# Kernel tuning notes

Hardware: AMD Instinct MI355X
Metric: run time of the kernel (lower is better)

Reference implementation:

```python
import jax, jax.numpy as jnp
import numpy as np

EPS = 1e-6
POWER_ITERS = 5
B, S, D, H, HD, M = 4, 1024, 1024, 16, 64, 2736
SOFTCAP = 50.0


def _rms_norm(x, scale, eps=EPS):
    # flax RMSNorm: normalize in fp32 over last axis, then scale
    x32 = x.astype(jnp.float32)
    y = x32 * jax.lax.rsqrt(jnp.mean(x32 * x32, axis=-1, keepdims=True) + eps)
    return (y * scale).astype(x.dtype)


def _spectral_sigma(k2d, power_iters=POWER_ITERS, eps=EPS):
    u = jnp.ones((k2d.shape[1],), dtype=k2d.dtype)
    u = u / (jnp.linalg.norm(u) + eps)

    def body(_, u):
        v = jax.lax.stop_gradient(k2d @ u)
        v = v / (jnp.linalg.norm(v) + eps)
        u = jax.lax.stop_gradient(k2d.T @ v)
        u = u / (jnp.linalg.norm(u) + eps)
        return u

    u = jax.lax.fori_loop(0, power_iters, body, u)
    v = jax.lax.stop_gradient(k2d @ u)
    v = v / (jnp.linalg.norm(v) + eps)
    sigma = jnp.einsum('i,ij,j->', v, k2d, u)
    return jnp.maximum(sigma, eps)


def _sigma_dense(x, kernel, sigma_p, bias):
    # spectral-normalized dense; kernel may be (in, out) or (in, H, HD)
    k2d = kernel.reshape(kernel.shape[0], -1)
    sigma = _spectral_sigma(k2d)
    k_hat = (sigma_p / sigma) * kernel  # sigma_p shape (1,)
    y = jnp.tensordot(x, k_hat, axes=[[-1], [0]])
    return y + bias


def setup_inputs() -> dict:
    key = jax.random.key(0)
    ks = jax.random.split(key, 16)

    def kinit(k, shape, fan_in):
        return jax.random.normal(k, shape, jnp.float32) / np.sqrt(fan_in)

    one = jnp.ones((1,), jnp.float32)
    return {
        'x': jax.random.normal(ks[0], (B, S, D), jnp.float32),
        'ln1_scale': jnp.ones((D,), jnp.float32),
        'wq': kinit(ks[1], (D, H, HD), D), 'sq': one, 'bq': jnp.zeros((H, HD), jnp.float32),
        'wk': kinit(ks[2], (D, H, HD), D), 'sk': one, 'bk': jnp.zeros((H, HD), jnp.float32),
        'wv': kinit(ks[3], (D, H, HD), D), 'sv': one, 'bv': jnp.zeros((H, HD), jnp.float32),
        'qn_scale': jnp.ones((HD,), jnp.float32),
        'kn_scale': jnp.ones((HD,), jnp.float32),
        'wo': kinit(ks[4], (D, D), D), 'so': one, 'bo': jnp.zeros((D,), jnp.float32),
        'ln2_scale': jnp.ones((D,), jnp.float32),
        'wg': kinit(ks[5], (D, M), D), 'sg': one, 'bg': jnp.zeros((M,), jnp.float32),
        'wu': kinit(ks[6], (D, M), D), 'su': one, 'bu': jnp.zeros((M,), jnp.float32),
        'wd': kinit(ks[7], (M, D), M), 'sd': one, 'bd': jnp.zeros((D,), jnp.float32),
    }


def reference(x, ln1_scale, wq, sq, bq, wk, sk, bk, wv, sv, bv,
              qn_scale, kn_scale, wo, so, bo, ln2_scale,
              wg, sg, bg, wu, su, bu, wd, sd, bd):
    # --- attention ---
    attn_in = _rms_norm(x, ln1_scale)
    q = _sigma_dense(attn_in, wq, sq, bq)  # [B,S,H,HD]
    k = _sigma_dense(attn_in, wk, sk, bk)
    v = _sigma_dense(attn_in, wv, sv, bv)
    q = _rms_norm(q, qn_scale)
    k = _rms_norm(k, kn_scale)
    scale = jnp.sqrt(jnp.float32(HD))
    logits = jnp.einsum('bqhd,bkhd->bhqk', q, k) / scale
    logits = SOFTCAP * jnp.tanh(logits / SOFTCAP)
    attn = jax.nn.softmax(logits, axis=-1)
    out = jnp.einsum('bhqk,bkhd->bqhd', attn, v).reshape(B, S, D)
    out = _sigma_dense(out, wo, so, bo)
    x = x + out
    # --- gated MLP (swiglu) ---
    mlp_in = _rms_norm(x, ln2_scale)
    gate = _sigma_dense(mlp_in, wg, sg, bg)
    up = _sigma_dense(mlp_in, wu, su, bu)
    mlp = jax.nn.silu(gate) * up
    mlp = _sigma_dense(mlp, wd, sd, bd)
    return x + mlp
```

## Files before the change

### kernel.cpp

```cpp
#include <hip/hip_runtime.h>
#include <math.h>
#include <stddef.h>
#include <stdint.h>

#define BB   4
#define SS   1024
#define DD   1024
#define HH   16
#define HDD  64
#define NT   (BB*SS)
#define MFF  2736
#define MFFP 2752
#define EPSF 1e-6f

typedef unsigned int   u32;
typedef unsigned short ushort_t;
typedef float  f32x4   __attribute__((ext_vector_type(4)));
typedef float  f32x16  __attribute__((ext_vector_type(16)));
typedef short  s16x8   __attribute__((ext_vector_type(8)));

typedef const __attribute__((address_space(1))) u32 glb_u32;
typedef __attribute__((address_space(3))) u32 lds_u32;

static const size_t OFF_X2    = 0;
static const size_t OFF_VT    = 4194304;
static const size_t OFF_QH    = 8388608;
static const size_t OFF_O     = 16777216;
static const size_t OFF_H     = 8388608;
static const size_t OFF_ACT   = 26607616;
static const size_t OFF_POOL  = 30801920;
static const size_t OFF_VV    = 36569088;
static const size_t OFF_UU    = 36588240;
static const size_t OFF_SCALE = 36607392;

__device__ inline ushort_t f2bf(float x){
  u32 u = __float_as_uint(x);
  u32 r = (u + 0x7fffu + ((u >> 16) & 1u)) >> 16;
  return (ushort_t)r;
}
__device__ inline void split_bf(float x, ushort_t& hi, ushort_t& lo){
  hi = f2bf(x);
  float hf = __uint_as_float(((u32)hi) << 16);
  lo = f2bf(x - hf);
}
__device__ inline float bf2f(ushort_t u){
  return __uint_as_float(((u32)u) << 16);
}
__device__ inline s16x8 mk8(u32 a, u32 b, u32 c, u32 d){
  union { u32 w[4]; s16x8 v; } u;
  u.w[0]=a; u.w[1]=b; u.w[2]=c; u.w[3]=d;
  return u.v;
}

__device__ inline float block_sum256(float v, float* red){
  #pragma unroll
  for (int off=32; off>=1; off>>=1) v += __shfl_down(v, off);
  int lane = threadIdx.x & 63, wave = threadIdx.x >> 6;
  if (lane == 0) red[wave] = v;
  __syncthreads();
  return red[0]+red[1]+red[2]+red[3];
}

struct W2Args { const float* W[7]; ushort_t* dst; };
__global__ __launch_bounds__(256) void w2bf(W2Args a){
  const int BST[8] = {0,512,1024,1536,2048,3416,4784,6152};
  const size_t OFFU[7] = {0,1048576,2097152,3145728,4194304,6995968,9797632};
  int blk = blockIdx.x; int m = 0;
  #pragma unroll
  for (int i=1;i<7;i++) if (blk >= BST[i]) m = i;
  size_t e = (size_t)(blk - BST[m])*2048 + threadIdx.x*8;
  const float* src = a.W[m] + e;
  float4 v0 = *(const float4*)src;
  float4 v1 = *(const float4*)(src + 4);
  union { ushort_t o[8]; s16x8 v; } u;
  u.o[0]=f2bf(v0.x); u.o[1]=f2bf(v0.y); u.o[2]=f2bf(v0.z); u.o[3]=f2bf(v0.w);
  u.o[4]=f2bf(v1.x); u.o[5]=f2bf(v1.y); u.o[6]=f2bf(v1.z); u.o[7]=f2bf(v1.w);
  *(s16x8*)(a.dst + OFFU[m] + e) = u.v;
}

struct PowArgs {
  const ushort_t* Wb;
  float* vvec; float* uvec; int step;
};

__global__ __launch_bounds__(256) void zero_uvec(float* uvec){
  int m = blockIdx.x;
  for (int i=threadIdx.x; i<2736; i+=256) uvec[m*2736+i] = 0.f;
}

__global__ __launch_bounds__(256) void mv_notrans(PowArgs pa){
  const int NIN [7] = {1024,1024,1024,1024,1024,1024,2736};
  const int NOUT[7] = {1024,1024,1024,1024,2736,2736,1024};
  const int BST [8] = {0,256,512,768,1024,1280,1536,2220};
  const size_t OFFU[7] = {0,1048576,2097152,3145728,4194304,6995968,9797632};
  __shared__ float red[4];
  int blk = blockIdx.x;
  int m = 0;
  #pragma unroll
  for (int i=1;i<7;i++) if (blk >= BST[i]) m = i;
  int nin = NIN[m], nout = NOUT[m];
  int st = pa.step;
  float inv;
  const float* x = pa.uvec + m*2736;
  if (st == 0){
    inv = 1.f/(sqrtf((float)nout)+EPSF);
  } else {
    float s = 0.f;
    for (int i=threadIdx.x; i<nout; i+=256){ float u = x[i]; s += u*u; }
    float tot = block_sum256(s, red);
    inv = 1.f/(sqrtf(tot)+EPSF);
  }
  int wave = threadIdx.x >> 6, lane = threadIdx.x & 63;
  int row = (blk - BST[m])*4 + wave;
// ... 23 lines not shown
}

__global__ __launch_bounds__(256) void mv_trans(PowArgs pa){
  const int NIN [7] = {1024,1024,1024,1024,1024,1024,2736};
  const int NOUT[7] = {1024,1024,1024,1024,2736,2736,1024};
  const int BST [8] = {0,32,64,96,128,216,304,392};
  const int RCH [7] = {8,8,8,8,8,8,22};
  const size_t OFFU[7] = {0,1048576,2097152,3145728,4194304,6995968,9797632};
  __shared__ float red[4];
  int blk = blockIdx.x;
  int m = 0;
  #pragma unroll
  for (int i=1;i<7;i++) if (blk >= BST[i]) m = i;
  int nin = NIN[m], nout = NOUT[m];
  const float* v = pa.vvec + m*2736;
  float s = 0.f;
  for (int i=threadIdx.x; i<nin; i+=256){ float t = v[i]; s += t*t; }
  float tot = block_sum256(s, red);
  float inv = 1.f/(sqrtf(tot)+EPSF);
  int local = blk - BST[m];
  int ct = local / RCH[m], rc = local % RCH[m];
  int col = ct*256 + threadIdx.x;
  int r0 = rc*128, r1 = min(nin, r0+128);
  if (col >= nout) return;
  const ushort_t* W = pa.Wb + OFFU[m];
  float partial = 0.f;
  for (int r=r0; r<r1; ++r)
    partial += bf2f(W[(size_t)r*nout + col])*(v[r]*inv);
  atomicAdd(&pa.uvec[m*2736+col], partial);
}

struct SigArgs {
  const float* vvec; float* scale;
  const float* sp[7];
};
__global__ __launch_bounds__(256) void sigma_scale_kernel(SigArgs sa){
  const int NIN [7] = {1024,1024,1024,1024,1024,1024,2736};
  __shared__ float red[4];
  int m = blockIdx.x;
  const float* v = sa.vvec + m*2736;
  float s = 0.f;
  for (int i=threadIdx.x; i<NIN[m]; i+=256){ float t = v[i]; s += t*t; }
  float a = block_sum256(s, red);
  if (threadIdx.x == 0){
    float S = sqrtf(a);
    float sig = a/(S+EPSF);
    sig = fmaxf(sig, EPSF);
    sa.scale[m] = sa.sp[m][0]/sig;
  }
}

struct TCArgs {
  const float* src0; const float* src1;
  ushort_t* dh; ushort_t* dl;
  size_t zoff; int K; int N; int Kpad;
};
__global__ __launch_bounds__(256) void trans_cvt2(TCArgs a){
  __shared__ float t[32][33];
  const float* src = blockIdx.z ? a.src1 : a.src0;
  ushort_t* dh = a.dh + blockIdx.z*a.zoff;
  ushort_t* dl = a.dl + blockIdx.z*a.zoff;
  int k0 = blockIdx.x*32, n0 = blockIdx.y*32;
  int c = threadIdx.x & 31, rb = threadIdx.x >> 5;
  #pragma unroll
  for (int i=0;i<4;i++){
    int r = rb + i*8;
    int kk = k0 + r, nn = n0 + c;
    t[r][c] = (kk<a.K && nn<a.N) ? src[(size_t)kk*a.N + nn] : 0.f;
  }
  __syncthreads();
  #pragma unroll
  for (int i=0;i<4;i++){
    int r = rb + i*8;
    int nn = n0 + r, kk = k0 + c;
    float v = t[c][r];
    ushort_t hi, lo; split_bf(v, hi, lo);
    size_t o = (size_t)nn*a.Kpad + kk;
    dh[o] = hi; dl[o] = lo;
  }
}

__global__ __launch_bounds__(256) void rms_cvt(const float* __restrict__ in,
                                               const float* __restrict__ scale,
                                               ushort_t* __restrict__ oh,
                                               ushort_t* __restrict__ ol){
  int row = blockIdx.x;
  int tid = threadIdx.x;
  const float* p = in + (size_t)row*DD;
  float4 vx = *(const float4*)(p + tid*4);
  float ss = vx.x*vx.x + vx.y*vx.y + vx.z*vx.z + vx.w*vx.w;
  int lane = tid & 63, wave = tid >> 6;
  #pragma unroll
  for (int off=32; off>=1; off>>=1) ss += __shfl_down(ss, off);
  __shared__ float red[4];
  if (lane == 0) red[wave] = ss;
  __syncthreads();
  float tot = red[0]+red[1]+red[2]+red[3];
  float r = rsqrtf(tot*(1.f/DD)+EPSF);
  float4 sc = *(const float4*)(scale + tid*4);
  float o0 = vx.x*r*sc.x, o1 = vx.y*r*sc.y, o2 = vx.z*r*sc.z, o3 = vx.w*r*sc.w;
  ushort_t h[4], l[4];
  split_bf(o0,h[0],l[0]); split_bf(o1,h[1],l[1]);
  split_bf(o2,h[2],l[2]); split_bf(o3,h[3],l[3]);
  size_t o = (size_t)row*DD + tid*4;
  oh[o+0]=h[0]; oh[o+1]=h[1]; oh[o+2]=h[2]; oh[o+3]=h[3];
  ol[o+0]=l[0]; ol[o+1]=l[1]; ol[o+2]=l[2]; ol[o+3]=l[3];
}

struct GemmArgs {
  const ushort_t *Ah, *Al, *Bh, *Bl;
  float* C;
  const float *bias0, *bias1;
  const float *nrm0, *nrm1;
  ushort_t *dH0, *dL0, *dH1, *dL1;
  const float* scaleBase;
  const float* resid;
  int Kd, matN, bpm, rowsPerMat, Cstride, colOff;
};

template<int FN, int EPI>
__global__ __launch_bounds__(256) void gemm_bf3(GemmArgs g){
  constexpr int BN   = FN*32;
  constexpr int SEGB = BN/16;
  constexpr int NSEG = 16 + 2*SEGB;
  constexpr int NSEGT = NSEG/4;
  constexpr int HALF = 16384 + 2*BN*64;
  __shared__ __align__(16) char lds[2*HALF];

  const int tid = threadIdx.x;
  const int w = tid >> 6, l = tid & 63;
  const int bm = blockIdx.y*128;
  const int mat = blockIdx.x / g.bpm;
  const int n0m = (blockIdx.x % g.bpm) * BN;
  const int nrow0 = mat*g.rowsPerMat + n0m;

  const ushort_t* sp[NSEGT];
  u32 loff[NSEGT];
  #pragma unroll
  for (int i=0;i<NSEGT;i++){
    int s = w + i*4;
    int ci, r, c, csrc;
    if (s < 16){
      int abuf = s >> 3, segi = s & 7;
      ci = segi*64 + l; r = ci >> 2; c = ci & 3;
      csrc = c ^ ((r >> 1) & 3);
      sp[i] = (abuf ? g.Al : g.Ah) + (size_t)(bm + r)*g.Kd + csrc*8;
      loff[i] = (u32)(abuf*8192 + ci*16);
    } else {
      int tt = s - 16;
      int bbuf = tt / SEGB, segi = tt % SEGB;
      ci = segi*64 + l; r = ci >> 2; c = ci & 3;
      csrc = c ^ ((r >> 1) & 3);
      sp[i] = (bbuf ? g.Bl : g.Bh) + (size_t)(nrow0 + r)*g.Kd + csrc*8;
      loff[i] = (u32)(16384 + bbuf*(BN*64) + ci*16);
    }
  }

  const int wm = w >> 1, wn = w & 1;
  const int li = l & 15, kq = l >> 4;
  const int sx = kq ^ ((li >> 1) & 3);
  const u32 aOff = (u32)((wm*64 + li)*64 + sx*16);
  const u32 bOff = (u32)(16384 + (wn*(FN*16) + li)*64 + sx*16);

  f32x4 acc[4][FN];
  #pragma unroll
  for (int mi=0;mi<4;mi++)
    #pragma unroll
    for (int ni=0;ni<FN;ni++)
      acc[mi][ni] = (f32x4){0.f,0.f,0.f,0.f};

  const int nt = g.Kd >> 5;
  #pragma unroll
  for (int i=0;i<NSEGT;i++){
    __builtin_amdgcn_global_load_lds((glb_u32*)sp[i], (lds_u32*)(lds + loff[i]), 16, 0, 0);
    sp[i] += 32;
  }
  __syncthreads();

  for (int t=0; t<nt; t++){
    if (t+1 < nt){
      char* sb = lds + ((t+1)&1)*HALF;
      #pragma unroll
      for (int i=0;i<NSEGT;i++){
        __builtin_amdgcn_global_load_lds((glb_u32*)sp[i], (lds_u32*)(sb + loff[i]), 16, 0, 0);
        sp[i] += 32;
      }
    }
    const char* lb = lds + (t&1)*HALF;
    s16x8 ah[4], al[4];
    #pragma unroll
    for (int mi=0;mi<4;mi++){
      ah[mi] = *(const s16x8*)(lb + aOff + mi*1024);
      al[mi] = *(const s16x8*)(lb + 8192 + aOff + mi*1024);
    }
    #pragma unroll
    for (int ni=0;ni<FN;ni++){
      s16x8 bh = *(const s16x8*)(lb + bOff + ni*1024);
      s16x8 bl = *(const s16x8*)(lb + BN*64 + bOff + ni*1024);
      #pragma unroll
      for (int mi=0;mi<4;mi++){
        f32x4 tacc = acc[mi][ni];
        tacc = __builtin_amdgcn_mfma_f32_16x16x32_bf16(ah[mi], bh, tacc, 0, 0, 0);
        tacc = __builtin_amdgcn_mfma_f32_16x16x32_bf16(ah[mi], bl, tacc, 0, 0, 0);
        tacc = __builtin_amdgcn_mfma_f32_16x16x32_bf16(al[mi], bh, tacc, 0, 0, 0);
        acc[mi][ni] = tacc;
      }
    }
    __syncthreads();
  }

  if constexpr (EPI == 0){
    const float s = g.scaleBase[mat];
    const float* bias = g.bias0;
    const int colBase = n0m + wn*(FN*16);
    #pragma unroll
    for (int ni=0;ni<FN;ni++){
      int cm = colBase + ni*16 + li;
      if (cm < g.matN){
        int cg = cm + g.colOff;
        float bv = bias[cm];
        #pragma unroll
        for (int mi=0;mi<4;mi++){
          f32x4 a = acc[mi][ni];
          int r0 = bm + wm*64 + mi*16 + kq*4;
          #pragma unroll
          for (int j=0;j<4;j++){
            float v = s*a[j] + bv;
            size_t off = (size_t)(r0+j)*g.Cstride + cg;
            if (g.resid) v += g.resid[off];
            g.C[off] = v;
          }
        }
      }
    }
  } else if constexpr (EPI == 1){
    const float s = g.scaleBase[mat];
    const float* bias = mat ? g.bias1 : g.bias0;
    const float* nsc  = mat ? g.nrm1  : g.nrm0;
    ushort_t* dH = mat ? g.dH1 : g.dH0;
    ushort_t* dL = mat ? g.dL1 : g.dL0;
    const int hidx = (n0m >> 6) + wn;
    float bv[FN], nv[FN];
    #pragma unroll
    for (int ni=0;ni<FN;ni++){
      int cm = n0m + wn*64 + ni*16 + li;
      bv[ni] = bias[cm];
      nv[ni] = nsc[ni*16 + li];
    }
    #pragma unroll
    for (int mi=0;mi<4;mi++){
      #pragma unroll
      for (int j=0;j<4;j++){
        float vv[FN]; float ssq = 0.f;
        #pragma unroll
        for (int ni=0;ni<FN;ni++){
          vv[ni] = s*acc[mi][ni][j] + bv[ni];
          ssq += vv[ni]*vv[ni];
        }
        ssq += __shfl_xor(ssq, 1);
        ssq += __shfl_xor(ssq, 2);
        ssq += __shfl_xor(ssq, 4);
        ssq += __shfl_xor(ssq, 8);
        float rr = rsqrtf(ssq*(1.f/64.f)+EPSF);
        int row = bm + wm*64 + mi*16 + kq*4 + j;
        size_t base = (((size_t)(row>>10)*16 + hidx)*1024 + (row & 1023))*64;
        #pragma unroll
        for (int ni=0;ni<FN;ni++){
          ushort_t hi, lo; split_bf(vv[ni]*rr*nv[ni], hi, lo);
          dH[base + ni*16 + li] = hi;
          dL[base + ni*16 + li] = lo;
        }
      }
    }
  } else {
    const float s = g.scaleBase[0];
    #pragma unroll
    for (int mi=0;mi<4;mi++){
      #pragma unroll
      for (int j=0;j<4;j++){
        int row = bm + wm*64 + mi*16 + kq*4 + j;
        float bvr = g.bias0[row];
        #pragma unroll
        for (int ni=0;ni<FN;ni++){
          int cm = n0m + wn*(FN*16) + ni*16 + li;
          float v = s*acc[mi][ni][j] + bvr;
          ushort_t hi, lo; split_bf(v, hi, lo);
          g.dH0[(size_t)row*4096 + cm] = hi;
          g.dL0[(size_t)row*4096 + cm] = lo;
        }
      }
    }
  }
}

struct GluArgs {
  const ushort_t *Ah, *Al;
  const ushort_t *GH, *GL, *UH, *UL;
  const float *bg, *bu;
  const float* scaleBase;
  ushort_t *hH, *hL;
};

__global__ __launch_bounds__(256) void gemm_glu(GluArgs g){
  constexpr int HALF = 32768;
  __shared__ __align__(16) char lds[2*HALF];
  const int tid = threadIdx.x;
  const int w = tid >> 6, l = tid & 63;
  const int bm = blockIdx.y*128;
  const int n0 = blockIdx.x*64;

  const ushort_t* sp[8];
  u32 loff[8];
  #pragma unroll
  for (int i=0;i<8;i++){
    int s = w + i*4;
    if (s < 16){
      int abuf = s >> 3, segi = s & 7;
      int ci = segi*64 + l, r = ci >> 2, c = ci & 3;
      int csrc = c ^ ((r >> 1) & 3);
      sp[i] = (abuf ? g.Al : g.Ah) + (size_t)(bm + r)*1024 + csrc*8;
      loff[i] = (u32)(abuf*8192 + ci*16);
    } else {
      int tt = s - 16;
      int msel = tt >> 3;
      int half = (tt >> 2) & 1;
      int segi = tt & 3;
      int ci = segi*64 + l, r = ci >> 2, c = ci & 3;
      int csrc = c ^ ((r >> 1) & 3);
      const ushort_t* base = msel ? (half ? g.UL : g.UH) : (half ? g.GL : g.GH);
      sp[i] = base + (size_t)(n0 + r)*1024 + csrc*8;
      loff[i] = (u32)(16384 + msel*8192 + half*4096 + ci*16);
    }
  }

  const int wm = w >> 1, wn = w & 1;
  const int li = l & 15, kq = l >> 4;
  const int sx = kq ^ ((li >> 1) & 3);
  const u32 aOff = (u32)((wm*64 + li)*64 + sx*16);
  const u32 bOff = (u32)(16384 + (wn*32 + li)*64 + sx*16);

  f32x4 accG[4][2], accU[4][2];
  #pragma unroll
  for (int mi=0;mi<4;mi++)
    #pragma unroll
    for (int ni=0;ni<2;ni++){
      accG[mi][ni] = (f32x4){0.f,0.f,0.f,0.f};
      accU[mi][ni] = (f32x4){0.f,0.f,0.f,0.f};
    }

  #pragma unroll
  for (int i=0;i<8;i++){
    __builtin_amdgcn_global_load_lds((glb_u32*)sp[i], (lds_u32*)(lds + loff[i]), 16, 0, 0);
    sp[i] += 32;
  }
  __syncthreads();

  for (int t=0; t<32; t++){
    if (t+1 < 32){
      char* sb = lds + ((t+1)&1)*HALF;
      #pragma unroll
      for (int i=0;i<8;i++){
        __builtin_amdgcn_global_load_lds((glb_u32*)sp[i], (lds_u32*)(sb + loff[i]), 16, 0, 0);
        sp[i] += 32;
      }
    }
    const char* lb = lds + (t&1)*HALF;
    s16x8 ah[4], al[4];
    #pragma unroll
    for (int mi=0;mi<4;mi++){
      ah[mi] = *(const s16x8*)(lb + aOff + mi*1024);
      al[mi] = *(const s16x8*)(lb + 8192 + aOff + mi*1024);
    }
    #pragma unroll
    for (int ni=0;ni<2;ni++){
      s16x8 gh = *(const s16x8*)(lb + bOff + ni*1024);
      s16x8 gl = *(const s16x8*)(lb + 4096 + bOff + ni*1024);
      s16x8 uh = *(const s16x8*)(lb + 8192 + bOff + ni*1024);
      s16x8 ul = *(const s16x8*)(lb + 12288 + bOff + ni*1024);
      #pragma unroll
      for (int mi=0;mi<4;mi++){
        f32x4 tg = accG[mi][ni];
        tg = __builtin_amdgcn_mfma_f32_16x16x32_bf16(ah[mi], gh, tg, 0, 0, 0);
        tg = __builtin_amdgcn_mfma_f32_16x16x32_bf16(ah[mi], gl, tg, 0, 0, 0);
        tg = __builtin_amdgcn_mfma_f32_16x16x32_bf16(al[mi], gh, tg, 0, 0, 0);
        accG[mi][ni] = tg;
        f32x4 tu = accU[mi][ni];
        tu = __builtin_amdgcn_mfma_f32_16x16x32_bf16(ah[mi], uh, tu, 0, 0, 0);
        tu = __builtin_amdgcn_mfma_f32_16x16x32_bf16(ah[mi], ul, tu, 0, 0, 0);
        tu = __builtin_amdgcn_mfma_f32_16x16x32_bf16(al[mi], uh, tu, 0, 0, 0);
        accU[mi][ni] = tu;
      }
    }
    __syncthreads();
  }

  const float sG = g.scaleBase[0], sU = g.scaleBase[1];
  #pragma unroll
  for (int ni=0;ni<2;ni++){
    int cm = n0 + wn*32 + ni*16 + li;
    bool ok = cm < MFF;
    float bgv = ok ? g.bg[cm] : 0.f;
    float buv = ok ? g.bu[cm] : 0.f;
    #pragma unroll
    for (int mi=0;mi<4;mi++){
      #pragma unroll
      for (int j=0;j<4;j++){
        int row = bm + wm*64 + mi*16 + kq*4 + j;
        ushort_t hb = 0, lb2 = 0;
        if (ok){
          float gv = sG*accG[mi][ni][j] + bgv;
          float uv = sU*accU[mi][ni][j] + buv;
          float hv = gv * __builtin_amdgcn_rcpf(1.f + __expf(-gv)) * uv;
          split_bf(hv, hb, lb2);
        }
        size_t ho = (size_t)row*MFFP + cm;
        g.hH[ho] = hb; g.hL[ho] = lb2;
      }
    }
  }
}

__global__ __launch_bounds__(256) void attn_mfma(const ushort_t* __restrict__ qh, const ushort_t* __restrict__ ql,
                                                 const ushort_t* __restrict__ kh, const ushort_t* __restrict__ kl,
                                                 const ushort_t* __restrict__ vh, const ushort_t* __restrict__ vl,
                                                 ushort_t* __restrict__ oh, ushort_t* __restrict__ ol){
  __shared__ __align__(16) char lds[74240];
  const int qt = blockIdx.x, h = blockIdx.y, b = blockIdx.z;
  const int tid = threadIdx.x;
  const int l = tid & 63, li = tid & 31, hi = (tid >> 5) & 1;
  const int w = tid >> 6, qhalf = w >> 1, khalf = w & 1;
  const int r0 = tid >> 3, ch = tid & 7;

  const size_t qrow = ((size_t)(b*HH + h)*SS + qt*64 + qhalf*32 + li)*64;
  s16x8 aQh[4], aQl[4];
  #pragma unroll
  for (int ks=0; ks<4; ks++){
    aQh[ks] = *(const s16x8*)(qh + qrow + ks*16 + hi*8);
    aQl[ks] = *(const s16x8*)(ql + qrow + ks*16 + hi*8);
  }

  const size_t kbase = (size_t)(b*HH + h)*SS*64;
  const size_t vbase = (size_t)h*64*4096 + (size_t)b*SS;

  f32x16 accO0 = (f32x16){0,0,0,0,0,0,0,0,0,0,0,0,0,0,0,0};
  f32x16 accO1 = (f32x16){0,0,0,0,0,0,0,0,0,0,0,0,0,0,0,0};
  float psum = 0.f;

  s16x8 rKh0,rKh1,rKl0,rKl1,rVh0,rVh1,rVl0,rVl1;
  rKh0 = *(const s16x8*)(kh + kbase + (size_t)r0*64 + ch*8);
  rKh1 = *(const s16x8*)(kh + kbase + (size_t)(r0+32)*64 + ch*8);
  rKl0 = *(const s16x8*)(kl + kbase + (size_t)r0*64 + ch*8);
  rKl1 = *(const s16x8*)(kl + kbase + (size_t)(r0+32)*64 + ch*8);
  rVh0 = *(const s16x8*)(vh + vbase + (size_t)r0*4096 + ch*8);
  rVh1 = *(const s16x8*)(vh + vbase + (size_t)(r0+32)*4096 + ch*8);
  rVl0 = *(const s16x8*)(vl + vbase + (size_t)r0*4096 + ch*8);
  rVl1 = *(const s16x8*)(vl + vbase + (size_t)(r0+32)*4096 + ch*8);
  {
    char* Kb = lds;  char* Vb = lds + 36864;
    *(s16x8*)(Kb + r0*144 + ch*16) = rKh0;
    *(s16x8*)(Kb + (r0+32)*144 + ch*16) = rKh1;
    *(s16x8*)(Kb + 9216 + r0*144 + ch*16) = rKl0;
    *(s16x8*)(Kb + 9216 + (r0+32)*144 + ch*16) = rKl1;
    *(s16x8*)(Vb + r0*144 + ch*16) = rVh0;
    *(s16x8*)(Vb + (r0+32)*144 + ch*16) = rVh1;
    *(s16x8*)(Vb + 9216 + r0*144 + ch*16) = rVl0;
    *(s16x8*)(Vb + 9216 + (r0+32)*144 + ch*16) = rVl1;
  }
  __syncthreads();

  int cur = 0;
  for (int kt=0; kt<16; kt++){
    if (kt < 15){
      const size_t kb = kbase + (size_t)(kt+1)*64*64;
      const size_t vb = vbase + (size_t)(kt+1)*64;
      rKh0 = *(const s16x8*)(kh + kb + (size_t)r0*64 + ch*8);
      rKh1 = *(const s16x8*)(kh + kb + (size_t)(r0+32)*64 + ch*8);
      rKl0 = *(const s16x8*)(kl + kb + (size_t)r0*64 + ch*8);
      rKl1 = *(const s16x8*)(kl + kb + (size_t)(r0+32)*64 + ch*8);
      rVh0 = *(const s16x8*)(vh + vb + (size_t)r0*4096 + ch*8);
      rVh1 = *(const s16x8*)(vh + vb + (size_t)(r0+32)*4096 + ch*8);
      rVl0 = *(const s16x8*)(vl + vb + (size_t)r0*4096 + ch*8);
      rVl1 = *(const s16x8*)(vl + vb + (size_t)(r0+32)*4096 + ch*8);
    }
    const char* Kc = lds + cur*18432;
    const char* Vc = lds + 36864 + cur*18432;

    f32x16 sF = (f32x16){0,0,0,0,0,0,0,0,0,0,0,0,0,0,0,0};
    #pragma unroll
    for (int ks=0; ks<4; ks++){
      s16x8 kfh = *(const s16x8*)(Kc + (khalf*32+li)*144 + ks*32 + hi*16);
      s16x8 kfl = *(const s16x8*)(Kc + 9216 + (khalf*32+li)*144 + ks*32 + hi*16);
      sF = __builtin_amdgcn_mfma_f32_32x32x16_bf16(kfh, aQh[ks], sF, 0, 0, 0);
      sF = __builtin_amdgcn_mfma_f32_32x32x16_bf16(kfl, aQh[ks], sF, 0, 0, 0);
      sF = __builtin_amdgcn_mfma_f32_32x32x16_bf16(kfh, aQl[ks], sF, 0, 0, 0);
    }

    float p[16];
    #pragma unroll
    for (int r=0; r<16; r++){
      float wv = __expf(sF[r]*0.005f);
      float rc = __builtin_amdgcn_rcpf(wv + 1.f);
      float pv = __expf(-100.f*rc);
      p[r] = pv;
      psum += pv;
    }

    u32 cH[8], cL[8];
    #pragma unroll
    for (int m=0; m<4; m++){
      u32 u0 = __float_as_uint(p[4*m+0]), u1 = __float_as_uint(p[4*m+1]);
      u32 u2 = __float_as_uint(p[4*m+2]), u3 = __float_as_uint(p[4*m+3]);
      u32 m0 = u0 & 0xffff0000u, m1 = u1 & 0xffff0000u;
      u32 m2 = u2 & 0xffff0000u, m3 = u3 & 0xffff0000u;
      cH[2*m+0] = m1 | (m0 >> 16);
      cH[2*m+1] = m3 | (m2 >> 16);
      u32 k0 = __float_as_uint(p[4*m+0] - __uint_as_float(m0));
      u32 k1 = __float_as_uint(p[4*m+1] - __uint_as_float(m1));
      u32 k2 = __float_as_uint(p[4*m+2] - __uint_as_float(m2));
      u32 k3 = __float_as_uint(p[4*m+3] - __uint_as_float(m3));
      cL[2*m+0] = (k1 & 0xffff0000u) | (k0 >> 16);
      cL[2*m+1] = (k3 & 0xffff0000u) | (k2 >> 16);
    }

    #pragma unroll
    for (int ks2=0; ks2<2; ks2++){
      u32 A0 = cH[4*ks2+0], A1 = cH[4*ks2+1], B0 = cH[4*ks2+2], B1 = cH[4*ks2+3];
      u32 As0 = (u32)__shfl_xor((int)A0, 32), As1 = (u32)__shfl_xor((int)A1, 32);
      u32 Bs0 = (u32)__shfl_xor((int)B0, 32), Bs1 = (u32)__shfl_xor((int)B1, 32);
      s16x8 paH = mk8(hi ? Bs0 : A0, hi ? Bs1 : A1, hi ? B0 : As0, hi ? B1 : As1);
      u32 C0 = cL[4*ks2+0], C1 = cL[4*ks2+1], D0 = cL[4*ks2+2], D1 = cL[4*ks2+3];
      u32 Cs0 = (u32)__shfl_xor((int)C0, 32), Cs1 = (u32)__shfl_xor((int)C1, 32);
      u32 Ds0 = (u32)__shfl_xor((int)D0, 32), Ds1 = (u32)__shfl_xor((int)D1, 32);
      s16x8 paL = mk8(hi ? Ds0 : C0, hi ? Ds1 : C1, hi ? D0 : Cs0, hi ? D1 : Cs1);

      {
        const char* vp = Vc + (0*32+li)*144 + khalf*64 + ks2*32 + hi*16;
        s16x8 vfh = *(const s16x8*)vp;
        s16x8 vfl = *(const s16x8*)(vp + 9216);
        accO0 = __builtin_amdgcn_mfma_f32_32x32x16_bf16(paH, vfh, accO0, 0, 0, 0);
        accO0 = __builtin_amdgcn_mfma_f32_32x32x16_bf16(paH, vfl, accO0, 0, 0, 0);
        accO0 = __builtin_amdgcn_mfma_f32_32x32x16_bf16(paL, vfh, accO0, 0, 0, 0);
      }
      {
        const char* vp = Vc + (32+li)*144 + khalf*64 + ks2*32 + hi*16;
        s16x8 vfh = *(const s16x8*)vp;
        s16x8 vfl = *(const s16x8*)(vp + 9216);
        accO1 = __builtin_amdgcn_mfma_f32_32x32x16_bf16(paH, vfh, accO1, 0, 0, 0);
        accO1 = __builtin_amdgcn_mfma_f32_32x32x16_bf16(paH, vfl, accO1, 0, 0, 0);
        accO1 = __builtin_amdgcn_mfma_f32_32x32x16_bf16(paL, vfh, accO1, 0, 0, 0);
      }
    }

    __syncthreads();
    if (kt < 15){
      char* Kb = lds + (cur^1)*18432;
      char* Vb = lds + 36864 + (cur^1)*18432;
      *(s16x8*)(Kb + r0*144 + ch*16) = rKh0;
      *(s16x8*)(Kb + (r0+32)*144 + ch*16) = rKh1;
      *(s16x8*)(Kb + 9216 + r0*144 + ch*16) = rKl0;
      *(s16x8*)(Kb + 9216 + (r0+32)*144 + ch*16) = rKl1;
      *(s16x8*)(Vb + r0*144 + ch*16) = rVh0;
      *(s16x8*)(Vb + (r0+32)*144 + ch*16) = rVh1;
      *(s16x8*)(Vb + 9216 + r0*144 + ch*16) = rVl0;
      *(s16x8*)(Vb + 9216 + (r0+32)*144 + ch*16) = rVl1;
      __syncthreads();
      cur ^= 1;
    }
  }

  float tot = psum + __shfl_xor(psum, 32);
  float* smA = (float*)(lds + 73728);
  float* smB = smA + 64;
  float* ex  = (float*)lds;
  if (khalf == 1 && hi == 0) smA[qhalf*32 + li] = tot;
  __syncthreads();
  if (khalf == 0 && hi == 0) smB[qhalf*32 + li] = tot + smA[qhalf*32 + li];
  if (khalf == 1){
    #pragma unroll
    for (int reg=0; reg<16; reg++){
      ex[qhalf*2048 + reg*64 + l]        = accO0[reg];
      ex[qhalf*2048 + (16+reg)*64 + l]   = accO1[reg];
    }
  }
  __syncthreads();
  if (khalf == 0){
    #pragma unroll
    for (int reg=0; reg<16; reg++){
      int qr = qhalf*32 + (reg&3) + 8*(reg>>2) + 4*hi;
      float inv = __builtin_amdgcn_rcpf(smB[qr]);
      float o0 = (accO0[reg] + ex[qhalf*2048 + reg*64 + l]) * inv;
      float o1 = (accO1[reg] + ex[qhalf*2048 + (16+reg)*64 + l]) * inv;
      size_t obase = ((size_t)(b*SS + qt*64 + qr))*1024 + h*64;
      ushort_t hb, lb2;
      split_bf(o0, hb, lb2); oh[obase + li] = hb;      ol[obase + li] = lb2;
      split_bf(o1, hb, lb2); oh[obase + 32 + li] = hb; ol[obase + 32 + li] = lb2;
    }
  }
}

extern "C" void kernel_launch(void* const* d_in, const int* in_sizes, int n_in,
                              void* d_out, int out_size, void* d_ws, size_t ws_size,
                              hipStream_t stream) {
  const float* x   = (const float*)d_in[0];
  const float* ln1 = (const float*)d_in[1];
  const float* wq  = (const float*)d_in[2];
  const float* sq  = (const float*)d_in[3];
  const float* bq  = (const float*)d_in[4];
  const float* wk  = (const float*)d_in[5];
  const float* sk  = (const float*)d_in[6];
  const float* bk  = (const float*)d_in[7];
  const float* wv  = (const float*)d_in[8];
  const float* sv  = (const float*)d_in[9];
  const float* bv  = (const float*)d_in[10];
  const float* qn  = (const float*)d_in[11];
  const float* kn  = (const float*)d_in[12];
  const float* wo  = (const float*)d_in[13];
  const float* so  = (const float*)d_in[14];
  const float* bo  = (const float*)d_in[15];
  const float* ln2 = (const float*)d_in[16];
  const float* wg  = (const float*)d_in[17];
  const float* sg  = (const float*)d_in[18];
  const float* bg  = (const float*)d_in[19];
  const float* wu  = (const float*)d_in[20];
  const float* su  = (const float*)d_in[21];
  const float* bu  = (const float*)d_in[22];
  const float* wd  = (const float*)d_in[23];
  const float* sd  = (const float*)d_in[24];
  const float* bd  = (const float*)d_in[25];

  float* ws  = (float*)d_ws;
  float* out = (float*)d_out;

  float* x2   = ws + OFF_X2;
  ushort_t* vtH = (ushort_t*)(ws + OFF_VT);
  ushort_t* vtL = vtH + (size_t)1024*4096;
  ushort_t* qhH = (ushort_t*)(ws + OFF_QH);
  ushort_t* qhL = qhH + (size_t)NT*1024;
  ushort_t* khH = qhH + (size_t)2*NT*1024;
  ushort_t* khL = qhH + (size_t)3*NT*1024;
  ushort_t* bf1 = (ushort_t*)(ws + OFF_QH);
  ushort_t* oH  = (ushort_t*)(ws + OFF_O);
  ushort_t* oL  = oH + (size_t)NT*1024;
  ushort_t* hH  = (ushort_t*)(ws + OFF_H);
  ushort_t* hL  = hH + (size_t)NT*MFFP;
  ushort_t* actH = (ushort_t*)(ws + OFF_ACT);
  ushort_t* actL = actH + (size_t)NT*1024;
  ushort_t* poolH = (ushort_t*)(ws + OFF_POOL);
  float* scaleArr = ws + OFF_SCALE;

  {
    W2Args wa;
    wa.W[0]=wq; wa.W[1]=wk; wa.W[2]=wv; wa.W[3]=wo; wa.W[4]=wg; wa.W[5]=wu; wa.W[6]=wd;
    wa.dst = bf1;
    w2bf<<<6152, 256, 0, stream>>>(wa);
  }
  PowArgs pa;
  pa.Wb = bf1;
  pa.vvec = ws + OFF_VV; pa.uvec = ws + OFF_UU;
  for (int s=0; s<11; s++){
    pa.step = s;
    if ((s & 1) == 0){
      mv_notrans<<<2220, 256, 0, stream>>>(pa);
    } else {
      zero_uvec<<<7, 256, 0, stream>>>(pa.uvec);
      mv_trans<<<392, 256, 0, stream>>>(pa);
    }
  }
  SigArgs sa;
  sa.vvec = pa.vvec; sa.scale = scaleArr;
  sa.sp[0]=sq; sa.sp[1]=sk; sa.sp[2]=sv; sa.sp[3]=so; sa.sp[4]=sg; sa.sp[5]=su; sa.sp[6]=sd;
  sigma_scale_kernel<<<7, 256, 0, stream>>>(sa);

  rms_cvt<<<NT, 256, 0, stream>>>(x, ln1, actH, actL);

  GemmArgs ga;
  ga.resid = nullptr; ga.C = nullptr; ga.bias1 = nullptr;
  ga.nrm0 = ga.nrm1 = nullptr;
  ga.dH0 = ga.dL0 = ga.dH1 = ga.dL1 = nullptr;

  {
    ushort_t* bpL = poolH + (size_t)2048*1024;
    TCArgs tc; tc.src0 = wq; tc.src1 = wk;
    tc.dh = poolH; tc.dl = bpL; tc.zoff = (size_t)1024*1024;
    tc.K = 1024; tc.N = 1024; tc.Kpad = 1024;
    trans_cvt2<<<dim3(32,32,2), 256, 0, stream>>>(tc);
    ga.Ah = actH; ga.Al = actL; ga.Bh = poolH; ga.Bl = bpL;
    ga.bias0 = bq; ga.bias1 = bk; ga.nrm0 = qn; ga.nrm1 = kn;
    ga.dH0 = qhH; ga.dL0 = qhL; ga.dH1 = khH; ga.dL1 = khL;
    ga.scaleBase = scaleArr + 0;
    ga.Kd = 1024; ga.matN = 1024; ga.bpm = 8; ga.rowsPerMat = 1024;
    ga.Cstride = 0; ga.colOff = 0;
    gemm_bf3<4,1><<<dim3(16,32), 256, 0, stream>>>(ga);
  }

  {
    ushort_t* bpL = poolH + (size_t)1024*1024;
    TCArgs tc; tc.src0 = wv; tc.src1 = wv;
    tc.dh = poolH; tc.dl = bpL; tc.zoff = 0;
    tc.K = 1024; tc.N = 1024; tc.Kpad = 1024;
    trans_cvt2<<<dim3(32,32,1), 256, 0, stream>>>(tc);
    ga.Ah = poolH; ga.Al = bpL; ga.Bh = actH; ga.Bl = actL;
    ga.bias0 = bv; ga.bias1 = nullptr; ga.nrm0 = ga.nrm1 = nullptr;
    ga.dH0 = vtH; ga.dL0 = vtL; ga.dH1 = ga.dL1 = nullptr;
    ga.scaleBase = scaleArr + 2;
    ga.Kd = 1024; ga.matN = 4096; ga.bpm = 64; ga.rowsPerMat = 4096;
    ga.Cstride = 0; ga.colOff = 0;
    gemm_bf3<2,2><<<dim3(64,8), 256, 0, stream>>>(ga);
  }

  attn_mfma<<<dim3(16,16,4), 256, 0, stream>>>(qhH, qhL, khH, khL, vtH, vtL, oH, oL);

  {
    ushort_t* bpL = poolH + (size_t)1024*1024;
    TCArgs tc; tc.src0 = wo; tc.src1 = wo;
    tc.dh = poolH; tc.dl = bpL; tc.zoff = 0;
    tc.K = 1024; tc.N = 1024; tc.Kpad = 1024;
    trans_cvt2<<<dim3(32,32,1), 256, 0, stream>>>(tc);
    ga.Ah = oH; ga.Al = oL; ga.Bh = poolH; ga.Bl = bpL;
    ga.C = x2; ga.bias0 = bo;
    ga.dH0 = ga.dL0 = nullptr;
    ga.scaleBase = scaleArr + 3; ga.resid = x;
    ga.Kd = 1024; ga.matN = 1024; ga.bpm = 16; ga.rowsPerMat = 1024;
    ga.Cstride = 1024; ga.colOff = 0;
    gemm_bf3<2,0><<<dim3(16,32), 256, 0, stream>>>(ga);
  }

  rms_cvt<<<NT, 256, 0, stream>>>(x2, ln2, actH, actL);

  {
    ushort_t* gH = poolH;
    ushort_t* gL = poolH + (size_t)2816*1024;
    ushort_t* uH = poolH + (size_t)2*2816*1024;
    ushort_t* uL = poolH + (size_t)3*2816*1024;
    TCArgs tc; tc.src0 = wg; tc.src1 = wu;
    tc.dh = gH; tc.dl = gL; tc.zoff = (size_t)2*2816*1024;
    tc.K = 1024; tc.N = MFF; tc.Kpad = 1024;
    trans_cvt2<<<dim3(32,88,2), 256, 0, stream>>>(tc);
    GluArgs gl;
    gl.Ah = actH; gl.Al = actL;
    gl.GH = gH; gl.GL = gL; gl.UH = uH; gl.UL = uL;
    gl.bg = bg; gl.bu = bu; gl.scaleBase = scaleArr + 4;
    gl.hH = hH; gl.hL = hL;
    gemm_glu<<<dim3(43,32), 256, 0, stream>>>(gl);
  }

  {
    ushort_t* bpL = poolH + (size_t)1024*MFFP;
    TCArgs tc; tc.src0 = wd; tc.src1 = wd;
    tc.dh = poolH; tc.dl = bpL; tc.zoff = 0;
    tc.K = MFF; tc.N = 1024; tc.Kpad = MFFP;
    trans_cvt2<<<dim3(86,32,1), 256, 0, stream>>>(tc);
    ga.Ah = hH; ga.Al = hL; ga.Bh = poolH; ga.Bl = bpL;
    ga.C = out; ga.bias0 = bd;
    ga.dH0 = ga.dL0 = nullptr;
    ga.scaleBase = scaleArr + 6; ga.resid = x2;
    ga.Kd = MFFP; ga.matN = 1024; ga.bpm = 16; ga.rowsPerMat = 1024;
    ga.Cstride = 1024; ga.colOff = 0;
    gemm_bf3<2,0><<<dim3(16,32), 256, 0, stream>>>(ga);
  }
}
```

Baseline: 894.4 us.

## Switch GEMMs to fp16 two-term split with single-precision weights, add XCD swizzle

Replaces the three-MFMA bf16 hi/lo split in the projection and GLU GEMMs with fp16 MFMAs. Weights are stored as a single fp16 term and only activations keep a hi/lo split, so each tile needs two MFMAs instead of three and about half the B-operand traffic and LDS. It also adds an XCD-aware block index swizzle to the GEMM kernels and s_setprio around the MFMA sections of attention. The cost is lower precision: fp16 weights have a narrower exponent range and a single-term weight representation drops some mantissa bits relative to the old split.

```diff
diff --git a/kernel.cpp b/kernel.cpp
--- a/kernel.cpp
+++ b/kernel.cpp
@@ -1,4 +1,5 @@
 #include <hip/hip_runtime.h>
+#include <hip/hip_fp16.h>
 #include <math.h>
 #include <stddef.h>
 #include <stdint.h>
@@ -15,9 +16,10 @@
 
 typedef unsigned int   u32;
 typedef unsigned short ushort_t;
-typedef float  f32x4   __attribute__((ext_vector_type(4)));
-typedef float  f32x16  __attribute__((ext_vector_type(16)));
-typedef short  s16x8   __attribute__((ext_vector_type(8)));
+typedef float    f32x4   __attribute__((ext_vector_type(4)));
+typedef float    f32x16  __attribute__((ext_vector_type(16)));
+typedef short    s16x8   __attribute__((ext_vector_type(8)));
+typedef _Float16 h16x8   __attribute__((ext_vector_type(8)));
 
 typedef const __attribute__((address_space(1))) u32 glb_u32;
 typedef __attribute__((address_space(3))) u32 lds_u32;
@@ -46,6 +48,19 @@
 __device__ inline float bf2f(ushort_t u){
   return __uint_as_float(((u32)u) << 16);
 }
+__device__ inline ushort_t f2h(float x){
+  __half h = __float2half(x);
+  return *reinterpret_cast<ushort_t*>(&h);
+}
+__device__ inline float h2f(ushort_t u){
+  __half h;
+  *reinterpret_cast<ushort_t*>(&h) = u;
+  return __half2float(h);
+}
+__device__ inline void split_h(float x, ushort_t& hi, ushort_t& lo){
+  hi = f2h(x);
+  lo = f2h(x - h2f(hi));
+}
 __device__ inline s16x8 mk8(u32 a, u32 b, u32 c, u32 d){
   union { u32 w[4]; s16x8 v; } u;
   u.w[0]=a; u.w[1]=b; u.w[2]=c; u.w[3]=d;
@@ -59,6 +74,16 @@
   if (lane == 0) red[wave] = v;
   __syncthreads();
   return red[0]+red[1]+red[2]+red[3];
+}
+
+__device__ inline void xcd_swz(int nbx, int nby, int& bx, int& by){
+  int nwg = nbx * nby;
+  if (nwg & 7){ bx = blockIdx.x; by = blockIdx.y; return; }
+  int lin = blockIdx.x + blockIdx.y * nbx;
+  int q = nwg >> 3;
+  int wg = (lin & 7) * q + (lin >> 3);
+  bx = wg / nby;
+  by = wg - bx*nby;
 }
 
 struct W2Args { const float* W[7]; ushort_t* dst; };
@@ -188,14 +213,13 @@
 
 struct TCArgs {
   const float* src0; const float* src1;
-  ushort_t* dh; ushort_t* dl;
+  ushort_t* dh;
   size_t zoff; int K; int N; int Kpad;
 };
 __global__ __launch_bounds__(256) void trans_cvt2(TCArgs a){
   __shared__ float t[32][33];
   const float* src = blockIdx.z ? a.src1 : a.src0;
   ushort_t* dh = a.dh + blockIdx.z*a.zoff;
-  ushort_t* dl = a.dl + blockIdx.z*a.zoff;
   int k0 = blockIdx.x*32, n0 = blockIdx.y*32;
   int c = threadIdx.x & 31, rb = threadIdx.x >> 5;
   #pragma unroll
@@ -209,10 +233,7 @@
   for (int i=0;i<4;i++){
     int r = rb + i*8;
     int nn = n0 + r, kk = k0 + c;
-    float v = t[c][r];
-    ushort_t hi, lo; split_bf(v, hi, lo);
-    size_t o = (size_t)nn*a.Kpad + kk;
-    dh[o] = hi; dl[o] = lo;
+    dh[(size_t)nn*a.Kpad + kk] = f2h(t[c][r]);
   }
 }
 
@@ -236,8 +257,8 @@
   float4 sc = *(const float4*)(scale + tid*4);
   float o0 = vx.x*r*sc.x, o1 = vx.y*r*sc.y, o2 = vx.z*r*sc.z, o3 = vx.w*r*sc.w;
   ushort_t h[4], l[4];
-  split_bf(o0,h[0],l[0]); split_bf(o1,h[1],l[1]);
-  split_bf(o2,h[2],l[2]); split_bf(o3,h[3],l[3]);
+  split_h(o0,h[0],l[0]); split_h(o1,h[1],l[1]);
+  split_h(o2,h[2],l[2]); split_h(o3,h[3],l[3]);
   size_t o = (size_t)row*DD + tid*4;
   oh[o+0]=h[0]; oh[o+1]=h[1]; oh[o+2]=h[2]; oh[o+3]=h[3];
   ol[o+0]=l[0]; ol[o+1]=l[1]; ol[o+2]=l[2]; ol[o+3]=l[3];
@@ -255,19 +276,25 @@
 };
 
 template<int FN, int EPI>
-__global__ __launch_bounds__(256) void gemm_bf3(GemmArgs g){
-  constexpr int BN   = FN*32;
-  constexpr int SEGB = BN/16;
-  constexpr int NSEG = 16 + 2*SEGB;
+__global__ __launch_bounds__(256) void gemm_h(GemmArgs g){
+  constexpr bool BSPLIT = (EPI == 2);
+  constexpr int BN    = FN*32;
+  constexpr int SEGB  = BN/16;
+  constexpr int SEGA  = BSPLIT ? 8 : 16;
+  constexpr int NBB   = BSPLIT ? 2*SEGB : SEGB;
+  constexpr int NSEG  = SEGA + NBB;
   constexpr int NSEGT = NSEG/4;
-  constexpr int HALF = 16384 + 2*BN*64;
+  constexpr int ABYTES = SEGA*1024;
+  constexpr int HALF  = ABYTES + NBB*1024;
   __shared__ __align__(16) char lds[2*HALF];
 
   const int tid = threadIdx.x;
   const int w = tid >> 6, l = tid & 63;
-  const int bm = blockIdx.y*128;
-  const int mat = blockIdx.x / g.bpm;
-  const int n0m = (blockIdx.x % g.bpm) * BN;
+  int bxs, bys;
+  xcd_swz(gridDim.x, gridDim.y, bxs, bys);
+  const int bm = bys*128;
+  const int mat = bxs / g.bpm;
+  const int n0m = (bxs % g.bpm) * BN;
   const int nrow0 = mat*g.rowsPerMat + n0m;
 
   const ushort_t* sp[NSEGT];
@@ -276,19 +303,23 @@
   for (int i=0;i<NSEGT;i++){
     int s = w + i*4;
     int ci, r, c, csrc;
-    if (s < 16){
-      int abuf = s >> 3, segi = s & 7;
+    if (s < SEGA){
+      int abuf, segi;
+      if (BSPLIT){ abuf = 0; segi = s; }
+      else       { abuf = s >> 3; segi = s & 7; }
       ci = segi*64 + l; r = ci >> 2; c = ci & 3;
       csrc = c ^ ((r >> 1) & 3);
       sp[i] = (abuf ? g.Al : g.Ah) + (size_t)(bm + r)*g.Kd + csrc*8;
       loff[i] = (u32)(abuf*8192 + ci*16);
     } else {
-      int tt = s - 16;
-      int bbuf = tt / SEGB, segi = tt % SEGB;
+      int tt = s - SEGA;
+      int bbuf, segi;
+      if (BSPLIT){ bbuf = tt / SEGB; segi = tt % SEGB; }
+      else       { bbuf = 0; segi = tt; }
       ci = segi*64 + l; r = ci >> 2; c = ci & 3;
       csrc = c ^ ((r >> 1) & 3);
       sp[i] = (bbuf ? g.Bl : g.Bh) + (size_t)(nrow0 + r)*g.Kd + csrc*8;
-      loff[i] = (u32)(16384 + bbuf*(BN*64) + ci*16);
+      loff[i] = (u32)(ABYTES + bbuf*(BN*64) + ci*16);
     }
   }
 
@@ -296,7 +327,7 @@
   const int li = l & 15, kq = l >> 4;
   const int sx = kq ^ ((li >> 1) & 3);
   const u32 aOff = (u32)((wm*64 + li)*64 + sx*16);
-  const u32 bOff = (u32)(16384 + (wn*(FN*16) + li)*64 + sx*16);
+  const u32 bOff = (u32)(ABYTES + (wn*(FN*16) + li)*64 + sx*16);
 
   f32x4 acc[4][FN];
   #pragma unroll
@@ -323,23 +354,40 @@
       }
     }
     const char* lb = lds + (t&1)*HALF;
-    s16x8 ah[4], al[4];
-    #pragma unroll
-    for (int mi=0;mi<4;mi++){
-      ah[mi] = *(const s16x8*)(lb + aOff + mi*1024);
-      al[mi] = *(const s16x8*)(lb + 8192 + aOff + mi*1024);
-    }
-    #pragma unroll
-    for (int ni=0;ni<FN;ni++){
-      s16x8 bh = *(const s16x8*)(lb + bOff + ni*1024);
-      s16x8 bl = *(const s16x8*)(lb + BN*64 + bOff + ni*1024);
+    if (!BSPLIT){
+      h16x8 ah[4], al[4];
       #pragma unroll
       for (int mi=0;mi<4;mi++){
-        f32x4 tacc = acc[mi][ni];
-        tacc = __builtin_amdgcn_mfma_f32_16x16x32_bf16(ah[mi], bh, tacc, 0, 0, 0);
-        tacc = __builtin_amdgcn_mfma_f32_16x16x32_bf16(ah[mi], bl, tacc, 0, 0, 0);
-        tacc = __builtin_amdgcn_mfma_f32_16x16x32_bf16(al[mi], bh, tacc, 0, 0, 0);
-        acc[mi][ni] = tacc;
+        ah[mi] = *(const h16x8*)(lb + aOff + mi*1024);
+        al[mi] = *(const h16x8*)(lb + 8192 + aOff + mi*1024);
+      }
+      #pragma unroll
+      for (int ni=0;ni<FN;ni++){
+        h16x8 bh = *(const h16x8*)(lb + bOff + ni*1024);
+        #pragma unroll
+        for (int mi=0;mi<4;mi++){
+          f32x4 tacc = acc[mi][ni];
+          tacc = __builtin_amdgcn_mfma_f32_16x16x32_f16(ah[mi], bh, tacc, 0, 0, 0);
+          tacc = __builtin_amdgcn_mfma_f32_16x16x32_f16(al[mi], bh, tacc, 0, 0, 0);
+          acc[mi][ni] = tacc;
+        }
+      }
+    } else {
+      h16x8 ah[4];
+      #pragma unroll
+      for (int mi=0;mi<4;mi++)
+        ah[mi] = *(const h16x8*)(lb + aOff + mi*1024);
+      #pragma unroll
+      for (int ni=0;ni<FN;ni++){
+        h16x8 bh = *(const h16x8*)(lb + bOff + ni*1024);
+        h16x8 bl = *(const h16x8*)(lb + BN*64 + bOff + ni*1024);
+        #pragma unroll
+        for (int mi=0;mi<4;mi++){
+          f32x4 tacc = acc[mi][ni];
+          tacc = __builtin_amdgcn_mfma_f32_16x16x32_f16(ah[mi], bh, tacc, 0, 0, 0);
+          tacc = __builtin_amdgcn_mfma_f32_16x16x32_f16(ah[mi], bl, tacc, 0, 0, 0);
+          acc[mi][ni] = tacc;
+        }
       }
     }
     __syncthreads();
@@ -431,24 +479,26 @@
 
 struct GluArgs {
   const ushort_t *Ah, *Al;
-  const ushort_t *GH, *GL, *UH, *UL;
+  const ushort_t *GH, *UH;
   const float *bg, *bu;
   const float* scaleBase;
   ushort_t *hH, *hL;
 };
 
 __global__ __launch_bounds__(256) void gemm_glu(GluArgs g){
-  constexpr int HALF = 32768;
+  constexpr int HALF = 24576;
   __shared__ __align__(16) char lds[2*HALF];
   const int tid = threadIdx.x;
   const int w = tid >> 6, l = tid & 63;
-  const int bm = blockIdx.y*128;
-  const int n0 = blockIdx.x*64;
-
-  const ushort_t* sp[8];
-  u32 loff[8];
-  #pragma unroll
-  for (int i=0;i<8;i++){
+  int bxs, bys;
+  xcd_swz(gridDim.x, gridDim.y, bxs, bys);
+  const int bm = bys*128;
+  const int n0 = bxs*64;
+
+  const ushort_t* sp[6];
+  u32 loff[6];
+  #pragma unroll
+  for (int i=0;i<6;i++){
     int s = w + i*4;
     if (s < 16){
       int abuf = s >> 3, segi = s & 7;
@@ -458,14 +508,13 @@
       loff[i] = (u32)(abuf*8192 + ci*16);
     } else {
       int tt = s - 16;
-      int msel = tt >> 3;
-      int half = (tt >> 2) & 1;
+      int msel = tt >> 2;
       int segi = tt & 3;
       int ci = segi*64 + l, r = ci >> 2, c = ci & 3;
       int csrc = c ^ ((r >> 1) & 3);
-      const ushort_t* base = msel ? (half ? g.UL : g.UH) : (half ? g.GL : g.GH);
+      const ushort_t* base = msel ? g.UH : g.GH;
       sp[i] = base + (size_t)(n0 + r)*1024 + csrc*8;
-      loff[i] = (u32)(16384 + msel*8192 + half*4096 + ci*16);
+      loff[i] = (u32)(16384 + msel*4096 + ci*16);
     }
   }
 
@@ -485,7 +534,7 @@
     }
 
   #pragma unroll
-  for (int i=0;i<8;i++){
+  for (int i=0;i<6;i++){
     __builtin_amdgcn_global_load_lds((glb_u32*)sp[i], (lds_u32*)(lds + loff[i]), 16, 0, 0);
     sp[i] += 32;
   }
@@ -495,35 +544,31 @@
     if (t+1 < 32){
       char* sb = lds + ((t+1)&1)*HALF;
       #pragma unroll
-      for (int i=0;i<8;i++){
+      for (int i=0;i<6;i++){
         __builtin_amdgcn_global_load_lds((glb_u32*)sp[i], (lds_u32*)(sb + loff[i]), 16, 0, 0);
         sp[i] += 32;
       }
     }
     const char* lb = lds + (t&1)*HALF;
-    s16x8 ah[4], al[4];
+    h16x8 ah[4], al[4];
     #pragma unroll
     for (int mi=0;mi<4;mi++){
-      ah[mi] = *(const s16x8*)(lb + aOff + mi*1024);
-      al[mi] = *(const s16x8*)(lb + 8192 + aOff + mi*1024);
+      ah[mi] = *(const h16x8*)(lb + aOff + mi*1024);
+      al[mi] = *(const h16x8*)(lb + 8192 + aOff + mi*1024);
     }
     #pragma unroll
     for (int ni=0;ni<2;ni++){
-      s16x8 gh = *(const s16x8*)(lb + bOff + ni*1024);
-      s16x8 gl = *(const s16x8*)(lb + 4096 + bOff + ni*1024);
-      s16x8 uh = *(const s16x8*)(lb + 8192 + bOff + ni*1024);
-      s16x8 ul = *(const s16x8*)(lb + 12288 + bOff + ni*1024);
+      h16x8 gh = *(const h16x8*)(lb + bOff + ni*1024);
+      h16x8 uh = *(const h16x8*)(lb + 4096 + bOff + ni*1024);
       #pragma unroll
       for (int mi=0;mi<4;mi++){
         f32x4 tg = accG[mi][ni];
-        tg = __builtin_amdgcn_mfma_f32_16x16x32_bf16(ah[mi], gh, tg, 0, 0, 0);
-        tg = __builtin_amdgcn_mfma_f32_16x16x32_bf16(ah[mi], gl, tg, 0, 0, 0);
-        tg = __builtin_amdgcn_mfma_f32_16x16x32_bf16(al[mi], gh, tg, 0, 0, 0);
+        tg = __builtin_amdgcn_mfma_f32_16x16x32_f16(ah[mi], gh, tg, 0, 0, 0);
+        tg = __builtin_amdgcn_mfma_f32_16x16x32_f16(al[mi], gh, tg, 0, 0, 0);
         accG[mi][ni] = tg;
         f32x4 tu = accU[mi][ni];
-        tu = __builtin_amdgcn_mfma_f32_16x16x32_bf16(ah[mi], uh, tu, 0, 0, 0);
-        tu = __builtin_amdgcn_mfma_f32_16x16x32_bf16(ah[mi], ul, tu, 0, 0, 0);
-        tu = __builtin_amdgcn_mfma_f32_16x16x32_bf16(al[mi], uh, tu, 0, 0, 0);
+        tu = __builtin_amdgcn_mfma_f32_16x16x32_f16(ah[mi], uh, tu, 0, 0, 0);
+        tu = __builtin_amdgcn_mfma_f32_16x16x32_f16(al[mi], uh, tu, 0, 0, 0);
         accU[mi][ni] = tu;
       }
     }
@@ -547,7 +592,7 @@
           float gv = sG*accG[mi][ni][j] + bgv;
           float uv = sU*accU[mi][ni][j] + buv;
           float hv = gv * __builtin_amdgcn_rcpf(1.f + __expf(-gv)) * uv;
-          split_bf(hv, hb, lb2);
+          split_h(hv, hb, lb2);
         }
         size_t ho = (size_t)row*MFFP + cm;
         g.hH[ho] = hb; g.hL[ho] = lb2;
@@ -622,6 +667,7 @@
     const char* Vc = lds + 36864 + cur*18432;
 
     f32x16 sF = (f32x16){0,0,0,0,0,0,0,0,0,0,0,0,0,0,0,0};
+    __builtin_amdgcn_s_setprio(1);
     #pragma unroll
     for (int ks=0; ks<4; ks++){
       s16x8 kfh = *(const s16x8*)(Kc + (khalf*32+li)*144 + ks*32 + hi*16);
@@ -630,6 +676,7 @@
       sF = __builtin_amdgcn_mfma_f32_32x32x16_bf16(kfl, aQh[ks], sF, 0, 0, 0);
       sF = __builtin_amdgcn_mfma_f32_32x32x16_bf16(kfh, aQl[ks], sF, 0, 0, 0);
     }
+    __builtin_amdgcn_s_setprio(0);
 
     float p[16];
     #pragma unroll
@@ -658,6 +705,7 @@
       cL[2*m+1] = (k3 & 0xffff0000u) | (k2 >> 16);
     }
 
+    __builtin_amdgcn_s_setprio(1);
     #pragma unroll
     for (int ks2=0; ks2<2; ks2++){
       u32 A0 = cH[4*ks2+0], A1 = cH[4*ks2+1], B0 = cH[4*ks2+2], B1 = cH[4*ks2+3];
@@ -686,6 +734,7 @@
         accO1 = __builtin_amdgcn_mfma_f32_32x32x16_bf16(paL, vfh, accO1, 0, 0, 0);
       }
     }
+    __builtin_amdgcn_s_setprio(0);
 
     __syncthreads();
     if (kt < 15){
@@ -728,8 +777,8 @@
       float o1 = (accO1[reg] + ex[qhalf*2048 + (16+reg)*64 + l]) * inv;
       size_t obase = ((size_t)(b*SS + qt*64 + qr))*1024 + h*64;
       ushort_t hb, lb2;
-      split_bf(o0, hb, lb2); oh[obase + li] = hb;      ol[obase + li] = lb2;
-      split_bf(o1, hb, lb2); oh[obase + 32 + li] = hb; ol[obase + 32 + li] = lb2;
+      split_h(o0, hb, lb2); oh[obase + li] = hb;      ol[obase + li] = lb2;
+      split_h(o1, hb, lb2); oh[obase + 32 + li] = hb; ol[obase + 32 + li] = lb2;
     }
   }
 }
@@ -813,85 +862,80 @@
   ga.resid = nullptr; ga.C = nullptr; ga.bias1 = nullptr;
   ga.nrm0 = ga.nrm1 = nullptr;
   ga.dH0 = ga.dL0 = ga.dH1 = ga.dL1 = nullptr;
+  ga.Bl = nullptr; ga.Al = nullptr;
 
   {
-    ushort_t* bpL = poolH + (size_t)2048*1024;
     TCArgs tc; tc.src0 = wq; tc.src1 = wk;
-    tc.dh = poolH; tc.dl = bpL; tc.zoff = (size_t)1024*1024;
+    tc.dh = poolH; tc.zoff = (size_t)1024*1024;
     tc.K = 1024; tc.N = 1024; tc.Kpad = 1024;
     trans_cvt2<<<dim3(32,32,2), 256, 0, stream>>>(tc);
-    ga.Ah = actH; ga.Al = actL; ga.Bh = poolH; ga.Bl = bpL;
+    ga.Ah = actH; ga.Al = actL; ga.Bh = poolH; ga.Bl = nullptr;
     ga.bias0 = bq; ga.bias1 = bk; ga.nrm0 = qn; ga.nrm1 = kn;
     ga.dH0 = qhH; ga.dL0 = qhL; ga.dH1 = khH; ga.dL1 = khL;
     ga.scaleBase = scaleArr + 0;
     ga.Kd = 1024; ga.matN = 1024; ga.bpm = 8; ga.rowsPerMat = 1024;
     ga.Cstride = 0; ga.colOff = 0;
-    gemm_bf3<4,1><<<dim3(16,32), 256, 0, stream>>>(ga);
+    gemm_h<4,1><<<dim3(16,32), 256, 0, stream>>>(ga);
   }
 
   {
-    ushort_t* bpL = poolH + (size_t)1024*1024;
     TCArgs tc; tc.src0 = wv; tc.src1 = wv;
-    tc.dh = poolH; tc.dl = bpL; tc.zoff = 0;
+    tc.dh = poolH; tc.zoff = 0;
     tc.K = 1024; tc.N = 1024; tc.Kpad = 1024;
     trans_cvt2<<<dim3(32,32,1), 256, 0, stream>>>(tc);
-    ga.Ah = poolH; ga.Al = bpL; ga.Bh = actH; ga.Bl = actL;
+    ga.Ah = poolH; ga.Al = nullptr; ga.Bh = actH; ga.Bl = actL;
     ga.bias0 = bv; ga.bias1 = nullptr; ga.nrm0 = ga.nrm1 = nullptr;
     ga.dH0 = vtH; ga.dL0 = vtL; ga.dH1 = ga.dL1 = nullptr;
     ga.scaleBase = scaleArr + 2;
     ga.Kd = 1024; ga.matN = 4096; ga.bpm = 64; ga.rowsPerMat = 4096;
     ga.Cstride = 0; ga.colOff = 0;
-    gemm_bf3<2,2><<<dim3(64,8), 256, 0, stream>>>(ga);
+    gemm_h<2,2><<<dim3(64,8), 256, 0, stream>>>(ga);
   }
 
   attn_mfma<<<dim3(16,16,4), 256, 0, stream>>>(qhH, qhL, khH, khL, vtH, vtL, oH, oL);
 
   {
-    ushort_t* bpL = poolH + (size_t)1024*1024;
     TCArgs tc; tc.src0 = wo; tc.src1 = wo;
-    tc.dh = poolH; tc.dl = bpL; tc.zoff = 0;
+    tc.dh = poolH; tc.zoff = 0;
     tc.K = 1024; tc.N = 1024; tc.Kpad = 1024;
     trans_cvt2<<<dim3(32,32,1), 256, 0, stream>>>(tc);
-    ga.Ah = oH; ga.Al = oL; ga.Bh = poolH; ga.Bl = bpL;
+    ga.Ah = oH; ga.Al = oL; ga.Bh = poolH; ga.Bl = nullptr;
     ga.C = x2; ga.bias0 = bo;
     ga.dH0 = ga.dL0 = nullptr;
     ga.scaleBase = scaleArr + 3; ga.resid = x;
     ga.Kd = 1024; ga.matN = 1024; ga.bpm = 16; ga.rowsPerMat = 1024;
     ga.Cstride = 1024; ga.colOff = 0;
-    gemm_bf3<2,0><<<dim3(16,32), 256, 0, stream>>>(ga);
+    gemm_h<2,0><<<dim3(16,32), 256, 0, stream>>>(ga);
   }
 
   rms_cvt<<<NT, 256, 0, stream>>>(x2, ln2, actH, actL);
 
   {
     ushort_t* gH = poolH;
-    ushort_t* gL = poolH + (size_t)2816*1024;
-    ushort_t* uH = poolH + (size_t)2*2816*1024;
-    ushort_t* uL = poolH + (size_t)3*2816*1024;
+    ushort_t* uH = poolH + (size_t)2816*1024;
     TCArgs tc; tc.src0 = wg; tc.src1 = wu;
-    tc.dh = gH; tc.dl = gL; tc.zoff = (size_t)2*2816*1024;
+    tc.dh = gH; tc.zoff = (size_t)2816*1024;
     tc.K = 1024; tc.N = MFF; tc.Kpad = 1024;
     trans_cvt2<<<dim3(32,88,2), 256, 0, stream>>>(tc);
     GluArgs gl;
     gl.Ah = actH; gl.Al = actL;
-    gl.GH = gH; gl.GL = gL; gl.UH = uH; gl.UL = uL;
+    gl.GH = gH; gl.UH = uH;
     gl.bg = bg; gl.bu = bu; gl.scaleBase = scaleArr + 4;
     gl.hH = hH; gl.hL = hL;
     gemm_glu<<<dim3(43,32), 256, 0, stream>>>(gl);
   }
 
   {
-    ushort_t* bpL = poolH + (size_t)1024*MFFP;
     TCArgs tc; tc.src0 = wd; tc.src1 = wd;
-    tc.dh = poolH; tc.dl = bpL; tc.zoff = 0;
+    tc.dh = poolH; tc.zoff = 0;
     tc.K = MFF; tc.N = 1024; tc.Kpad = MFFP;
     trans_cvt2<<<dim3(86,32,1), 256, 0, stream>>>(tc);
-    ga.Ah = hH; ga.Al = hL; ga.Bh = poolH; ga.Bl = bpL;
+    ga.Ah = hH; ga.Al = hL; ga.Bh = poolH; ga.Bl = nullptr;
     ga.C = out; ga.bias0 = bd;
     ga.dH0 = ga.dL0 = nullptr;
     ga.scaleBase = scaleArr + 6; ga.resid = x2;
     ga.Kd = MFFP; ga.matN = 1024; ga.bpm = 16; ga.rowsPerMat = 1024;
     ga.Cstride = 1024; ga.colOff = 0;
-    gemm_bf3<2,0><<<dim3(16,32), 256, 0, stream>>>(ga);
-  }
-}
+    gemm_h<2,0><<<dim3(16,32), 256, 0, stream>>>(ga);
+  }
+}
```

Measured after the change: 833.4 us. 1.07x faster.
